# Kernel optimization log

Hardware: AMD Instinct MI355X
Metric: run time of the kernel (lower is better)

## Reference

```python
import jax, jax.numpy as jnp
import numpy as np

B, S, D_MODEL = 64, 2048, 512
NUM_UNITS = 512
WINDOW = 128  # attention_window_size


def setup_inputs() -> dict:
    key = jax.random.key(0)
    k1, k2, k3, k4, k5 = jax.random.split(key, 5)
    query = jax.random.normal(k1, (B, D_MODEL), dtype=jnp.float32)
    keys = jax.random.normal(k2, (B, S, D_MODEL), dtype=jnp.float32)
    key_lengths = jax.random.randint(k3, (B,), 0, 256, dtype=jnp.int32)
    Wq = jax.random.normal(k4, (NUM_UNITS, D_MODEL), dtype=jnp.float32) * 0.04
    wp = jax.random.normal(k5, (1, NUM_UNITS), dtype=jnp.float32) * 0.04
    return {"query": query, "keys": keys, "key_lengths": key_lengths, "Wq": Wq, "wp": wp}


def reference(query, keys, key_lengths, Wq, wp):
    # dot score: [B, S]
    score = jnp.einsum('bd,bsd->bs', query, keys)
    weight = jax.nn.softmax(score, axis=-1)

    # predictive local alignment
    L = key_lengths.astype(jnp.float32)[:, None]                      # [B, 1]
    activated = jnp.tanh(query @ Wq.T)                                # [B, num_units]
    sig = jax.nn.sigmoid(activated @ wp.T)                            # [B, 1]
    p = L * sig                                                       # [B, 1] predicted alignment point

    # window bounds via .int() truncation toward zero
    start = jnp.trunc(p - WINDOW).astype(jnp.int32)                   # [B, 1]
    end = jnp.trunc(p + WINDOW).astype(jnp.int32)                     # [B, 1]

    # gaussian factor (note: original uses L - p, a per-row scalar; 2*std = WINDOW)
    g = jnp.exp(-((L - p) ** 2) / WINDOW)                             # [B, 1]
    weight = weight * g                                               # [B, S]

    # per-row dynamic window gather + weighted sum, done as masked reduction
    pos = jnp.arange(S, dtype=jnp.int32)[None, :]                     # [1, S]
    mask = (pos >= start) & (pos < end)                               # [B, S]
    w = jnp.where(mask, weight, jnp.zeros((), dtype=weight.dtype))
    total_context = jnp.einsum('bs,bsd->bd', w, keys)                 # [B, d]
    return total_context, score
```

## Files before the change

kernel.cpp:

```cpp
#include <hip/hip_runtime.h>
#include <math.h>

#define BB 64
#define SS 2048
#define DD 512
#define NU 512
#define WIN 128
#define NSLICE 4
#define PART_OFF 1024

__device__ __forceinline__ float wave_reduce_sum(float v) {
    #pragma unroll
    for (int off = 32; off > 0; off >>= 1)
        v += __shfl_down(v, off, 64);
    return v;
}

__device__ __forceinline__ float wave_reduce_max(float v) {
    #pragma unroll
    for (int off = 32; off > 0; off >>= 1)
        v = fmaxf(v, __shfl_down(v, off, 64));
    return v;
}

__device__ __forceinline__ float dot4(const float4 a, const float4 b) {
    return a.x * b.x + a.y * b.y + a.z * b.z + a.w * b.w;
}

__global__ __launch_bounds__(256, 4) void score_p_kernel(const float* __restrict__ query,
                                                         const float* __restrict__ keys,
                                                         const int* __restrict__ key_lengths,
                                                         const float* __restrict__ Wq,
                                                         const float* __restrict__ wp,
                                                         float* __restrict__ score,
                                                         float* __restrict__ ws) {
    const int t    = threadIdx.x;
    const int wave = t >> 6;
    const int lane = t & 63;
    const int g    = lane >> 4;
    const int w    = lane & 15;

    if (blockIdx.x < BB) {
        const int b = blockIdx.x;
        __shared__ float act[NU];
        __shared__ float wsum[4];

        const float4* qv = (const float4*)(query + b * DD);
        const float4 q0 = qv[w],       q1 = qv[16 + w],  q2 = qv[32 + w],  q3 = qv[48 + w];
        const float4 q4 = qv[64 + w],  q5 = qv[80 + w],  q6 = qv[96 + w],  q7 = qv[112 + w];

        #pragma unroll 2
        for (int pass = 0; pass < 32; ++pass) {
            const int u = pass * 16 + wave * 4 + g;
            const float4* rv = (const float4*)(Wq + (size_t)u * DD);
            const float4 k0 = rv[w],       k1 = rv[16 + w],  k2 = rv[32 + w],  k3 = rv[48 + w];
            const float4 k4 = rv[64 + w],  k5 = rv[80 + w],  k6 = rv[96 + w],  k7 = rv[112 + w];
            const float s0 = dot4(k0, q0), s1 = dot4(k1, q1), s2 = dot4(k2, q2), s3 = dot4(k3, q3);
            const float s4 = dot4(k4, q4), s5 = dot4(k5, q5), s6 = dot4(k6, q6), s7 = dot4(k7, q7);
            float acc = ((s0 + s1) + (s2 + s3)) + ((s4 + s5) + (s6 + s7));
            #pragma unroll
            for (int m = 1; m < 16; m <<= 1)
                acc += __shfl_xor(acc, m, 64);
            if (w == 0) act[u] = tanhf(acc);
        }
        __syncthreads();

        float sv = act[t] * wp[t] + act[t + 256] * wp[t + 256];
        sv = wave_reduce_sum(sv);
        if (lane == 0) wsum[wave] = sv;
        __syncthreads();

        if (t == 0) {
            const float s = wsum[0] + wsum[1] + wsum[2] + wsum[3];
            const float sig = 1.0f / (1.0f + expf(-s));
            const float L = (float)key_lengths[b];
            const float p = L * sig;
            const int start = (int)(p - (float)WIN);
            const int end   = (int)(p + (float)WIN);
            const float diff = L - p;
            const float gg = expf(-(diff * diff) / (float)WIN);
            ws[b] = gg;
            ((int*)ws)[BB + b]     = start;
            ((int*)ws)[2 * BB + b] = end;
        }
    } else {
        const int bid   = blockIdx.x - BB;
        const int b     = bid >> 5;
        const int chunk = bid & 31;
        const int r0    = chunk * 64 + wave * 16;

        const float4* qv = (const float4*)(query + b * DD);
        const float4 q0 = qv[w],       q1 = qv[16 + w],  q2 = qv[32 + w],  q3 = qv[48 + w];
        const float4 q4 = qv[64 + w],  q5 = qv[80 + w],  q6 = qv[96 + w],  q7 = qv[112 + w];

        const float4* kb = (const float4*)(keys + (size_t)b * SS * DD);

        const float4* rv = kb + (size_t)(r0 + g) * (DD / 4);
        float4 k0 = rv[w],       k1 = rv[16 + w],  k2 = rv[32 + w],  k3 = rv[48 + w];
        float4 k4 = rv[64 + w],  k5 = rv[80 + w],  k6 = rv[96 + w],  k7 = rv[112 + w];

        #pragma unroll
        for (int p = 0; p < 4; ++p) {
            float4 n0, n1, n2, n3, n4, n5, n6, n7;
            if (p < 3) {
                const float4* nv = kb + (size_t)(r0 + (p + 1) * 4 + g) * (DD / 4);
                n0 = nv[w];       n1 = nv[16 + w];  n2 = nv[32 + w];  n3 = nv[48 + w];
                n4 = nv[64 + w];  n5 = nv[80 + w];  n6 = nv[96 + w];  n7 = nv[112 + w];
            }
            const float s0 = dot4(k0, q0), s1 = dot4(k1, q1), s2 = dot4(k2, q2), s3 = dot4(k3, q3);
            const float s4 = dot4(k4, q4), s5 = dot4(k5, q5), s6 = dot4(k6, q6), s7 = dot4(k7, q7);
            float acc = ((s0 + s1) + (s2 + s3)) + ((s4 + s5) + (s6 + s7));
            #pragma unroll
            for (int m = 1; m < 16; m <<= 1)
                acc += __shfl_xor(acc, m, 64);
            if (w == 0) score[b * SS + r0 + p * 4 + g] = acc;
            if (p < 3) {
                k0 = n0; k1 = n1; k2 = n2; k3 = n3;
                k4 = n4; k5 = n5; k6 = n6; k7 = n7;
            }
        }
    }
}

__global__ __launch_bounds__(512) void ctxA_kernel(const float* __restrict__ keys,
                                                   const float* __restrict__ score,
                                                   const float* __restrict__ ws,
                                                   float* __restrict__ part) {
    const int b     = blockIdx.x;
    const int slice = blockIdx.y;
    const int t     = threadIdx.x;
    const int wave  = t >> 6;
    const int lane  = t & 63;

    __shared__ float w_lds[72];
    __shared__ float redm[8], reds[8];
    __shared__ float4 part_l[3][128];

    const float* srow = score + b * SS;

    const float4 v0 = ((const float4*)srow)[t];
    float m = fmaxf(fmaxf(v0.x, v0.y), fmaxf(v0.z, v0.w));
    m = wave_reduce_max(m);
    if (lane == 0) redm[wave] = m;
    __syncthreads();
    float mx = redm[0];
    #pragma unroll
    for (int i = 1; i < 8; ++i) mx = fmaxf(mx, redm[i]);

    float sum = expf(v0.x - mx) + expf(v0.y - mx) + expf(v0.z - mx) + expf(v0.w - mx);
    sum = wave_reduce_sum(sum);
    if (lane == 0) reds[wave] = sum;
    __syncthreads();
    float tot = 0.f;
    #pragma unroll
    for (int i = 0; i < 8; ++i) tot += reds[i];
    const float inv = 1.0f / tot;

    const float gg   = ws[b];
    const int start  = ((const int*)ws)[BB + b];
    const int end    = ((const int*)ws)[2 * BB + b];
    const int s_lo   = max(start, 0);
    const int s_hi   = min(end, SS);
    const int width  = s_hi - s_lo;
    const int sliceN = (width + NSLICE - 1) / NSLICE;
    const int i_lo   = slice * sliceN;
    const int i_hi   = min(i_lo + sliceN, width);
    const int n      = i_hi - i_lo;

    for (int i = t; i < n; i += 512)
        w_lds[i] = expf(srow[s_lo + i_lo + i] - mx) * inv * gg;
    __syncthreads();

    const int myrow = t >> 7;
    const int c4    = t & 127;
    const float4* kb = (const float4*)(keys + ((size_t)b * SS + s_lo + i_lo) * DD);

    float4 acc = make_float4(0.f, 0.f, 0.f, 0.f);
    for (int i = myrow; i < n; i += 4) {
        const float4 k = kb[(size_t)i * (DD / 4) + c4];
        const float wg = w_lds[i];
        acc.x += wg * k.x; acc.y += wg * k.y; acc.z += wg * k.z; acc.w += wg * k.w;
    }

    if (myrow) part_l[myrow - 1][c4] = acc;
    __syncthreads();
    if (myrow == 0) {
        #pragma unroll
        for (int r = 0; r < 3; ++r) {
            const float4 o = part_l[r][c4];
            acc.x += o.x; acc.y += o.y; acc.z += o.z; acc.w += o.w;
        }
        ((float4*)part)[((size_t)b * NSLICE + slice) * 128 + c4] = acc;
    }
}

__global__ __launch_bounds__(512) void ctxB_kernel(const float* __restrict__ part,
                                                   float* __restrict__ ctx) {
    const int b = blockIdx.x;
    const int d = threadIdx.x;
    float s = 0.f;
    #pragma unroll
    for (int sl = 0; sl < NSLICE; ++sl)
        s += part[((size_t)b * NSLICE + sl) * DD + d];
    ctx[b * DD + d] = s;
}

extern "C" void kernel_launch(void* const* d_in, const int* in_sizes, int n_in,
                              void* d_out, int out_size, void* d_ws, size_t ws_size,
                              hipStream_t stream) {
    const float* query       = (const float*)d_in[0];
    const float* keys        = (const float*)d_in[1];
    const int*   key_lengths = (const int*)d_in[2];
    const float* Wq          = (const float*)d_in[3];
    const float* wp          = (const float*)d_in[4];

    float* ctx   = (float*)d_out;
    float* score = (float*)d_out + BB * DD;
    float* ws    = (float*)d_ws;
    float* part  = (float*)d_ws + PART_OFF;

    hipLaunchKernelGGL(score_p_kernel, dim3(BB + BB * 32), dim3(256), 0, stream,
                       query, keys, key_lengths, Wq, wp, score, ws);
    hipLaunchKernelGGL(ctxA_kernel, dim3(BB, NSLICE), dim3(512), 0, stream,
                       keys, score, ws, part);
    hipLaunchKernelGGL(ctxB_kernel, dim3(BB), dim3(512), 0, stream,
                       part, ctx);
}
```

Baseline: 63.70 us.

## Compute per-chunk softmax max/sum in score kernel, merge partials in context kernel

The score kernel now keeps each 64-row chunk's scores in shared memory and writes a local max and sum of exponentials per chunk to the workspace. The context kernel merges these 32 partial statistics with an online-softmax rescale instead of rereading the full 2048-score row and doing two block-wide reductions. This removes a score-row read and two block barriers per context block. In exchange the score kernel gains a barrier, extra exponentials, and a larger workspace layout.

```diff
diff --git a/kernel.cpp b/kernel.cpp
--- a/kernel.cpp
+++ b/kernel.cpp
@@ -7,7 +7,12 @@
 #define NU 512
 #define WIN 128
 #define NSLICE 4
-#define PART_OFF 1024
+#define G_OFF   0
+#define ST_OFF  64
+#define EN_OFF  128
+#define M_OFF   256
+#define S_OFF   (256 + BB * 32)
+#define PART_OFF 8192
 
 __device__ __forceinline__ float wave_reduce_sum(float v) {
     #pragma unroll
@@ -79,15 +84,16 @@
             const int end   = (int)(p + (float)WIN);
             const float diff = L - p;
             const float gg = expf(-(diff * diff) / (float)WIN);
-            ws[b] = gg;
-            ((int*)ws)[BB + b]     = start;
-            ((int*)ws)[2 * BB + b] = end;
+            ws[G_OFF + b] = gg;
+            ((int*)ws)[ST_OFF + b] = start;
+            ((int*)ws)[EN_OFF + b] = end;
         }
     } else {
         const int bid   = blockIdx.x - BB;
         const int b     = bid >> 5;
         const int chunk = bid & 31;
         const int r0    = chunk * 64 + wave * 16;
+        __shared__ float sc_l[64];
 
         const float4* qv = (const float4*)(query + b * DD);
         const float4 q0 = qv[w],       q1 = qv[16 + w],  q2 = qv[32 + w],  q3 = qv[48 + w];
@@ -113,10 +119,25 @@
             #pragma unroll
             for (int m = 1; m < 16; m <<= 1)
                 acc += __shfl_xor(acc, m, 64);
-            if (w == 0) score[b * SS + r0 + p * 4 + g] = acc;
+            if (w == 0) {
+                score[b * SS + r0 + p * 4 + g] = acc;
+                sc_l[wave * 16 + p * 4 + g] = acc;
+            }
             if (p < 3) {
                 k0 = n0; k1 = n1; k2 = n2; k3 = n3;
                 k4 = n4; k5 = n5; k6 = n6; k7 = n7;
+            }
+        }
+        __syncthreads();
+
+        if (t < 64) {
+            const float v = sc_l[t];
+            float m = wave_reduce_max(v);
+            const float mloc = __shfl(m, 0, 64);
+            const float ssum = wave_reduce_sum(expf(v - mloc));
+            if (t == 0) {
+                ws[M_OFF + b * 32 + chunk] = mloc;
+                ws[S_OFF + b * 32 + chunk] = ssum;
             }
         }
     }
@@ -133,32 +154,24 @@
     const int lane  = t & 63;
 
     __shared__ float w_lds[72];
-    __shared__ float redm[8], reds[8];
+    __shared__ float stat_l[2];
     __shared__ float4 part_l[3][128];
 
-    const float* srow = score + b * SS;
-
-    const float4 v0 = ((const float4*)srow)[t];
-    float m = fmaxf(fmaxf(v0.x, v0.y), fmaxf(v0.z, v0.w));
-    m = wave_reduce_max(m);
-    if (lane == 0) redm[wave] = m;
+    if (wave == 0) {
+        const float mi = (lane < 32) ? ws[M_OFF + b * 32 + lane] : -INFINITY;
+        float m = wave_reduce_max(mi);
+        const float mx0 = __shfl(m, 0, 64);
+        const float si = (lane < 32) ? ws[S_OFF + b * 32 + lane] * expf(mi - mx0) : 0.f;
+        float s = wave_reduce_sum(si);
+        if (lane == 0) { stat_l[0] = mx0; stat_l[1] = 1.0f / s; }
+    }
     __syncthreads();
-    float mx = redm[0];
-    #pragma unroll
-    for (int i = 1; i < 8; ++i) mx = fmaxf(mx, redm[i]);
-
-    float sum = expf(v0.x - mx) + expf(v0.y - mx) + expf(v0.z - mx) + expf(v0.w - mx);
-    sum = wave_reduce_sum(sum);
-    if (lane == 0) reds[wave] = sum;
-    __syncthreads();
-    float tot = 0.f;
-    #pragma unroll
-    for (int i = 0; i < 8; ++i) tot += reds[i];
-    const float inv = 1.0f / tot;
-
-    const float gg   = ws[b];
-    const int start  = ((const int*)ws)[BB + b];
-    const int end    = ((const int*)ws)[2 * BB + b];
+    const float mx  = stat_l[0];
+    const float inv = stat_l[1];
+
+    const float gg   = ws[G_OFF + b];
+    const int start  = ((const int*)ws)[ST_OFF + b];
+    const int end    = ((const int*)ws)[EN_OFF + b];
     const int s_lo   = max(start, 0);
     const int s_hi   = min(end, SS);
     const int width  = s_hi - s_lo;
@@ -167,6 +180,7 @@
     const int i_hi   = min(i_lo + sliceN, width);
     const int n      = i_hi - i_lo;
 
+    const float* srow = score + b * SS;
     for (int i = t; i < n; i += 512)
         w_lds[i] = expf(srow[s_lo + i_lo + i] - mx) * inv * gg;
     __syncthreads();
```

Measured after the change: 62.63 us. Within noise of the previous version (-1.7%).
